# Kernel tuning notes

Hardware: AMD Instinct MI355X
Metric: run time of the kernel (lower is better)

The kernel has to match this reference:

```python
import jax, jax.numpy as jnp
import numpy as np

IN_DIM, HID_DIM, OUT_DIM = 1024, 2048, 1024
DEG1, DEG2 = 8, 8
BATCH = 16384


def cheby_kan_layer(x, coeffs):
    """x: [b, i]; coeffs: [i, o, d+1] -> [b, o].
    Per-feature min-max normalize over batch to [-1,1], Chebyshev recurrence, contract."""
    degree = coeffs.shape[-1] - 1
    mn = jnp.min(x, axis=0, keepdims=True)
    mx = jnp.max(x, axis=0, keepdims=True)
    x = 2.0 * (x - mn) / (mx - mn) - 1.0
    Ts = [jnp.ones_like(x)]
    if degree > 0:
        Ts.append(x)
    for _ in range(2, degree + 1):
        Ts.append(2.0 * x * Ts[-1] - Ts[-2])
    cheby = jnp.stack(Ts, axis=-1)  # [b, i, d+1]
    return jnp.einsum('bid,iod->bo', cheby, coeffs)


def setup_inputs() -> dict:
    key = jax.random.key(0)
    k1, k2, k3 = jax.random.split(key, 3)
    x = jax.random.normal(k1, (BATCH, IN_DIM), dtype=jnp.float32)
    # kaiming-uniform-ish init for coeffs
    b1 = float(np.sqrt(6.0 / IN_DIM))
    b2 = float(np.sqrt(6.0 / HID_DIM))
    coeffs1 = jax.random.uniform(k2, (IN_DIM, HID_DIM, DEG1 + 1), dtype=jnp.float32, minval=-b1, maxval=b1)
    coeffs2 = jax.random.uniform(k3, (HID_DIM, OUT_DIM, DEG2 + 1), dtype=jnp.float32, minval=-b2, maxval=b2)
    return {"x": x, "coeffs1": coeffs1, "coeffs2": coeffs2}


def reference(x, coeffs1, coeffs2):
    h = cheby_kan_layer(x, coeffs1)
    y = cheby_kan_layer(h, coeffs2)
    return y
```

## Files before the change

### kernel.cpp

```cpp
#include <hip/hip_runtime.h>
#include <hip/hip_bf16.h>
#include <stdint.h>


constexpr int BATCH   = 16384;
constexpr int IN_DIM  = 1024;
constexpr int HID_DIM = 2048;
constexpr int OUT_DIM = 1024;
#define DP1 9

using bf16_t = __hip_bfloat16;

typedef __attribute__((ext_vector_type(4))) float f32x4;
typedef __attribute__((ext_vector_type(8))) short s16x8;

static __device__ __forceinline__ unsigned int f2bf_u(float f) {
  union { __hip_bfloat16 h; unsigned short u; } cv;
  cv.h = __float2bfloat16(f);
  return (unsigned int)cv.u;
}

template <typename T>
__global__ void kan_minmax_partial(const T* __restrict__ x, int rows, int cols,
                                   float* __restrict__ mnp, float* __restrict__ mxp) {
  const int c  = blockIdx.x * 64 + (threadIdx.x & 63);
  const int rg = threadIdx.x >> 6;
  const int P  = gridDim.y;
  const int chunk = rows / P;
  const int r0 = blockIdx.y * chunk;
  float mn = 1e30f, mx = -1e30f;
  for (int r = r0 + rg; r < r0 + chunk; r += 4) {
    float v = (float)x[(size_t)r * cols + c];
    mn = fminf(mn, v); mx = fmaxf(mx, v);
  }
  __shared__ float smn[256], smx[256];
  smn[threadIdx.x] = mn; smx[threadIdx.x] = mx;
  __syncthreads();
  if (rg == 0) {
    int t = threadIdx.x;
    mn = fminf(fminf(smn[t], smn[t + 64]), fminf(smn[t + 128], smn[t + 192]));
    mx = fmaxf(fmaxf(smx[t], smx[t + 64]), fmaxf(smx[t + 128], smx[t + 192]));
    mnp[(size_t)blockIdx.y * cols + c] = mn;
    mxp[(size_t)blockIdx.y * cols + c] = mx;
  }
}

__global__ void kan_minmax_finalize(const float* __restrict__ mnp, const float* __restrict__ mxp,
                                    int cols, int P, float* __restrict__ s, float* __restrict__ t) {
  int c = blockIdx.x * blockDim.x + threadIdx.x;
  if (c >= cols) return;
  float mn = 1e30f, mx = -1e30f;
  for (int p = 0; p < P; ++p) {
    mn = fminf(mn, mnp[(size_t)p * cols + c]);
    mx = fmaxf(mx, mxp[(size_t)p * cols + c]);
  }
  float inv = 2.0f / (mx - mn);
  s[c] = inv;
  t[c] = -mn * inv - 1.0f;
}

__global__ void kan_repack(const float* __restrict__ coeffs, int I, int O,
                           bf16_t* __restrict__ Bp) {
  const int NIB = I / 32;
  const int slab = blockIdx.x;
  const int d  = slab % 9;
  const int t2 = slab / 9;
  const int ib = t2 % NIB;
  const int ntile = t2 / NIB;
  for (int c = threadIdx.x; c < 1024; c += 256) {
    const int l16  = c & 15;
    const int quad = (c >> 4) & 3;
    const int ng   = c >> 6;
    const int o = ntile * 256 + ng * 16 + l16;
    const int ibase = ib * 32 + quad * 8;
    unsigned int pk[4];
#pragma unroll
    for (int q = 0; q < 4; ++q) {
      float v0 = coeffs[((size_t)(ibase + 2 * q + 0) * O + o) * DP1 + d];
      float v1 = coeffs[((size_t)(ibase + 2 * q + 1) * O + o) * DP1 + d];
      pk[q] = f2bf_u(v0) | (f2bf_u(v1) << 16);
    }
    *reinterpret_cast<uint4*>(reinterpret_cast<char*>(Bp) +
        ((size_t)slab * 8192 + (size_t)c * 8) * 2) = make_uint4(pk[0], pk[1], pk[2], pk[3]);
  }
}

template <typename AT, typename OT>
__launch_bounds__(256, 2)
__global__ void kan_cheby_gemm(const AT* __restrict__ X, const bf16_t* __restrict__ Bp,
                               const float* __restrict__ sc, const float* __restrict__ tc,
                               OT* __restrict__ out, int I, int N) {
  __shared__ __align__(16) short Als[4096];
  __shared__ __align__(16) short Bls[2][8192];

  const int m0   = blockIdx.x * 128;
  const int n0   = blockIdx.y * 256;
  const int tid  = threadIdx.x;
  const int lane = tid & 63;
  const int wave = tid >> 6;
  const int wr   = wave >> 1;
  const int wc   = wave & 1;
  const int wm4  = wr * 4;
  const int wn16 = wc * 8;
  const int quad = lane >> 4;
  const int l16  = lane & 15;

  const int ma = tid & 127;
  const int hf = tid >> 7;

  const int NIB = I / 32;
  const int nstage = NIB * 9;
  const size_t slab_base = (size_t)blockIdx.y * NIB * 9 * 8192;

  auto dma_b = [&](int ss) {
    const char* g = reinterpret_cast<const char*>(Bp + slab_base + (size_t)ss * 8192) +
                    wave * 4096 + lane * 16;
    char* l = reinterpret_cast<char*>(&Bls[ss & 1][0]) + wave * 4096;
#pragma unroll
    for (int t = 0; t < 4; ++t)
      __builtin_amdgcn_global_load_lds(
          (const __attribute__((address_space(1))) void*)(g + t * 1024),
          (__attribute__((address_space(3))) void*)(l + t * 1024), 16, 0, 0);
  };

  f32x4 acc[4][8] = {};
  float xv[16], Tm1[16], Tm2[16];
#pragma unroll
  for (int j = 0; j < 16; ++j) { xv[j] = 0.f; Tm1[j] = 0.f; Tm2[j] = 0.f; }

  dma_b(0);

  int ib = 0, d = 0;
  for (int s = 0; s < nstage; ++s) {
    __syncthreads();

    if (d == 0) {
      const int fbase = ib * 32 + hf * 16;
      const AT* xp = X + (size_t)(m0 + ma) * I + fbase;
      if constexpr (sizeof(AT) == 4) {
        const float4* p4 = reinterpret_cast<const float4*>(xp);
#pragma unroll
        for (int v = 0; v < 4; ++v) {
          float4 f = p4[v];
          xv[4 * v + 0] = f.x; xv[4 * v + 1] = f.y;
          xv[4 * v + 2] = f.z; xv[4 * v + 3] = f.w;
        }
      } else {
        const uint4* p4 = reinterpret_cast<const uint4*>(xp);
#pragma unroll
        for (int v = 0; v < 2; ++v) {
          uint4 u = p4[v];
          unsigned int wv[4] = {u.x, u.y, u.z, u.w};
#pragma unroll
          for (int q = 0; q < 4; ++q) {
            xv[8 * v + 2 * q + 0] = __uint_as_float(wv[q] << 16);
            xv[8 * v + 2 * q + 1] = __uint_as_float(wv[q] & 0xffff0000u);
          }
        }
      }
      const float4* sp = reinterpret_cast<const float4*>(sc + fbase);
      const float4* tp = reinterpret_cast<const float4*>(tc + fbase);
#pragma unroll
      for (int v = 0; v < 4; ++v) {
        float4 sv = sp[v], tv4 = tp[v];
        xv[4 * v + 0] = fmaf(xv[4 * v + 0], sv.x, tv4.x);
        xv[4 * v + 1] = fmaf(xv[4 * v + 1], sv.y, tv4.y);
        xv[4 * v + 2] = fmaf(xv[4 * v + 2], sv.z, tv4.z);
        xv[4 * v + 3] = fmaf(xv[4 * v + 3], sv.w, tv4.w);
      }
    }

    {
      float tv[16];
      if (d == 0) {
#pragma unroll
        for (int j = 0; j < 16; ++j) tv[j] = 1.0f;
      } else if (d == 1) {
#pragma unroll
        for (int j = 0; j < 16; ++j) tv[j] = xv[j];
      } else {
#pragma unroll
        for (int j = 0; j < 16; ++j) tv[j] = fmaf(2.0f * xv[j], Tm1[j], -Tm2[j]);
      }
#pragma unroll
      for (int j = 0; j < 16; ++j) { Tm2[j] = Tm1[j]; Tm1[j] = tv[j]; }

      unsigned int pk[8];
#pragma unroll
      for (int q = 0; q < 8; ++q)
        pk[q] = f2bf_u(tv[2 * q]) | (f2bf_u(tv[2 * q + 1]) << 16);
      char* b = reinterpret_cast<char*>(Als) +
                (ma >> 4) * 1024 + hf * 512 + (ma & 15) * 16;
      *reinterpret_cast<uint4*>(b)       = make_uint4(pk[0], pk[1], pk[2], pk[3]);
      *reinterpret_cast<uint4*>(b + 256) = make_uint4(pk[4], pk[5], pk[6], pk[7]);
    }

    __syncthreads();

    if (s + 1 < nstage) dma_b(s + 1);

    {
      const char* Ab = reinterpret_cast<const char*>(Als) + lane * 16;
      const char* Bb = reinterpret_cast<const char*>(&Bls[s & 1][0]) + lane * 16;
      s16x8 fa[4], fb[8];
#pragma unroll
      for (int mt = 0; mt < 4; ++mt)
        fa[mt] = *reinterpret_cast<const s16x8*>(Ab + (wm4 + mt) * 1024);
#pragma unroll
      for (int nt = 0; nt < 8; ++nt)
        fb[nt] = *reinterpret_cast<const s16x8*>(Bb + (wn16 + nt) * 1024);
#pragma unroll
      for (int mt = 0; mt < 4; ++mt)
#pragma unroll
        for (int nt = 0; nt < 8; ++nt)
          acc[mt][nt] = __builtin_amdgcn_mfma_f32_16x16x32_bf16(
              fa[mt], fb[nt], acc[mt][nt], 0, 0, 0);
    }

    if (++d == DP1) { d = 0; ++ib; }
  }

#pragma unroll
  for (int mt = 0; mt < 4; ++mt) {
#pragma unroll
    for (int nt = 0; nt < 8; ++nt) {
      const int n = n0 + wc * 128 + nt * 16 + l16;
#pragma unroll
      for (int r = 0; r < 4; ++r) {
        const int m = m0 + wr * 64 + mt * 16 + quad * 4 + r;
        float v = acc[mt][nt][r];
        if constexpr (sizeof(OT) == 4)
          out[(size_t)m * N + n] = v;
        else
          out[(size_t)m * N + n] = __float2bfloat16(v);
      }
    }
  }
}

extern "C" void kernel_launch(void* const* d_in, const int* in_sizes, int n_in,
                              void* d_out, int out_size, void* d_ws, size_t ws_size,
                              hipStream_t stream) {
  const float* x  = (const float*)d_in[0];
  const float* c1 = (const float*)d_in[1];
  const float* c2 = (const float*)d_in[2];
  float* out = (float*)d_out;

  char* ws = (char*)d_ws;
  size_t off = 0;
  auto take = [&](size_t n) -> char* {
    char* p = ws + off;
    off += (n + 255) & ~(size_t)255;
    return p;
  };
  bf16_t* Bp1 = (bf16_t*)take((size_t)HID_DIM * IN_DIM  * DP1 * 2);
  bf16_t* Bp2 = (bf16_t*)take((size_t)OUT_DIM * HID_DIM * DP1 * 2);
  bf16_t* h   = (bf16_t*)take((size_t)BATCH * HID_DIM * 2);
  float* s1  = (float*)take(IN_DIM  * 4);
  float* t1  = (float*)take(IN_DIM  * 4);
  float* s2  = (float*)take(HID_DIM * 4);
  float* t2  = (float*)take(HID_DIM * 4);
  float* mnp = (float*)take((size_t)16 * HID_DIM * 4);
  float* mxp = (float*)take((size_t)16 * HID_DIM * 4);

  kan_minmax_partial<float><<<dim3(IN_DIM / 64, 16), 256, 0, stream>>>(x, BATCH, IN_DIM, mnp, mxp);
  kan_minmax_finalize<<<dim3(IN_DIM / 256), 256, 0, stream>>>(mnp, mxp, IN_DIM, 16, s1, t1);
  kan_repack<<<dim3((HID_DIM / 256) * (IN_DIM / 32) * 9), 256, 0, stream>>>(c1, IN_DIM, HID_DIM, Bp1);
  kan_repack<<<dim3((OUT_DIM / 256) * (HID_DIM / 32) * 9), 256, 0, stream>>>(c2, HID_DIM, OUT_DIM, Bp2);
  kan_cheby_gemm<float, bf16_t><<<dim3(BATCH / 128, HID_DIM / 256), 256, 0, stream>>>(
      x, Bp1, s1, t1, h, IN_DIM, HID_DIM);

  kan_minmax_partial<bf16_t><<<dim3(HID_DIM / 64, 16), 256, 0, stream>>>(h, BATCH, HID_DIM, mnp, mxp);
  kan_minmax_finalize<<<dim3(HID_DIM / 256), 256, 0, stream>>>(mnp, mxp, HID_DIM, 16, s2, t2);
  kan_cheby_gemm<bf16_t, float><<<dim3(BATCH / 128, OUT_DIM / 256), 256, 0, stream>>>(
      h, Bp2, s2, t2, out, HID_DIM, OUT_DIM);
}
```

Measured before the change: 2.216 ms.

## Double-buffer A tile, prefetch X, single barrier per stage, and coalesce repack

The GEMM now double-buffers the Chebyshev A tile in LDS and builds stage s+1's A operand (and issues the B DMA) before running stage s's MFMAs. This cuts two barriers per stage to one and overlaps the basis computation with the matrix work. Raw X loads for the next feature block are prefetched into registers, and the bf16 conversion uses a vector convertvector. The repack kernel reads all 9 degrees per coefficient contiguously, where it previously did 9 strided passes. In exchange it uses more LDS and registers, which may hurt the 2-blocks-per-CU occupancy.

```diff
diff --git a/kernel.cpp b/kernel.cpp
--- a/kernel.cpp
+++ b/kernel.cpp
@@ -13,6 +13,8 @@
 
 typedef __attribute__((ext_vector_type(4))) float f32x4;
 typedef __attribute__((ext_vector_type(8))) short s16x8;
+typedef __attribute__((ext_vector_type(16))) float f32x16;
+typedef __attribute__((ext_vector_type(16))) __bf16 bf16x16;
 
 static __device__ __forceinline__ unsigned int f2bf_u(float f) {
   union { __hip_bfloat16 h; unsigned short u; } cv;
@@ -62,26 +64,32 @@
 __global__ void kan_repack(const float* __restrict__ coeffs, int I, int O,
                            bf16_t* __restrict__ Bp) {
   const int NIB = I / 32;
-  const int slab = blockIdx.x;
-  const int d  = slab % 9;
-  const int t2 = slab / 9;
-  const int ib = t2 % NIB;
-  const int ntile = t2 / NIB;
+  const int ib = blockIdx.x % NIB;
+  const int ntile = blockIdx.x / NIB;
+  const size_t slab0 = (size_t)(ntile * NIB + ib) * 9 * 8192;
   for (int c = threadIdx.x; c < 1024; c += 256) {
     const int l16  = c & 15;
     const int quad = (c >> 4) & 3;
     const int ng   = c >> 6;
     const int o = ntile * 256 + ng * 16 + l16;
     const int ibase = ib * 32 + quad * 8;
-    unsigned int pk[4];
-#pragma unroll
-    for (int q = 0; q < 4; ++q) {
-      float v0 = coeffs[((size_t)(ibase + 2 * q + 0) * O + o) * DP1 + d];
-      float v1 = coeffs[((size_t)(ibase + 2 * q + 1) * O + o) * DP1 + d];
-      pk[q] = f2bf_u(v0) | (f2bf_u(v1) << 16);
-    }
-    *reinterpret_cast<uint4*>(reinterpret_cast<char*>(Bp) +
-        ((size_t)slab * 8192 + (size_t)c * 8) * 2) = make_uint4(pk[0], pk[1], pk[2], pk[3]);
+    float v[8][9];
+#pragma unroll
+    for (int q = 0; q < 8; ++q) {
+      const float* rp = coeffs + ((size_t)(ibase + q) * O + o) * DP1;
+#pragma unroll
+      for (int d = 0; d < 9; ++d) v[q][d] = rp[d];
+    }
+#pragma unroll
+    for (int d = 0; d < 9; ++d) {
+      unsigned int pk[4];
+#pragma unroll
+      for (int q = 0; q < 4; ++q)
+        pk[q] = f2bf_u(v[2 * q][d]) | (f2bf_u(v[2 * q + 1][d]) << 16);
+      *reinterpret_cast<uint4*>(reinterpret_cast<char*>(Bp) +
+          (slab0 + (size_t)d * 8192 + (size_t)c * 8) * 2) =
+          make_uint4(pk[0], pk[1], pk[2], pk[3]);
+    }
   }
 }
 
@@ -90,11 +98,10 @@
 __global__ void kan_cheby_gemm(const AT* __restrict__ X, const bf16_t* __restrict__ Bp,
                                const float* __restrict__ sc, const float* __restrict__ tc,
                                OT* __restrict__ out, int I, int N) {
-  __shared__ __align__(16) short Als[4096];
+  __shared__ __align__(16) short Als[2][4096];
   __shared__ __align__(16) short Bls[2][8192];
 
   const int m0   = blockIdx.x * 128;
-  const int n0   = blockIdx.y * 256;
   const int tid  = threadIdx.x;
   const int lane = tid & 63;
   const int wave = tid >> 6;
@@ -123,84 +130,95 @@
           (__attribute__((address_space(3))) void*)(l + t * 1024), 16, 0, 0);
   };
 
+  uint4 rq[4];
+  auto load_raw = [&](int ibx) {
+    const char* xp = reinterpret_cast<const char*>(
+        X + (size_t)(m0 + ma) * I + ibx * 32 + hf * 16);
+    if constexpr (sizeof(AT) == 4) {
+      rq[0] = *reinterpret_cast<const uint4*>(xp +  0);
+      rq[1] = *reinterpret_cast<const uint4*>(xp + 16);
+      rq[2] = *reinterpret_cast<const uint4*>(xp + 32);
+      rq[3] = *reinterpret_cast<const uint4*>(xp + 48);
+    } else {
+      rq[0] = *reinterpret_cast<const uint4*>(xp +  0);
+      rq[1] = *reinterpret_cast<const uint4*>(xp + 16);
+    }
+  };
+
+  f32x16 xv, Tm1, Tm2;
+#pragma unroll
+  for (int j = 0; j < 16; ++j) { xv[j] = 0.f; Tm1[j] = 0.f; Tm2[j] = 0.f; }
+
+  auto unpack_norm = [&](int ibx) {
+    const int fbase = ibx * 32 + hf * 16;
+    float rv[16];
+    const unsigned int* w = reinterpret_cast<const unsigned int*>(rq);
+    if constexpr (sizeof(AT) == 4) {
+#pragma unroll
+      for (int j = 0; j < 16; ++j) rv[j] = __uint_as_float(w[j]);
+    } else {
+#pragma unroll
+      for (int q = 0; q < 8; ++q) {
+        rv[2 * q + 0] = __uint_as_float(w[q] << 16);
+        rv[2 * q + 1] = __uint_as_float(w[q] & 0xffff0000u);
+      }
+    }
+    const float4* sp = reinterpret_cast<const float4*>(sc + fbase);
+    const float4* tp = reinterpret_cast<const float4*>(tc + fbase);
+#pragma unroll
+    for (int v = 0; v < 4; ++v) {
+      float4 s4 = sp[v], t4 = tp[v];
+      xv[4 * v + 0] = fmaf(rv[4 * v + 0], s4.x, t4.x);
+      xv[4 * v + 1] = fmaf(rv[4 * v + 1], s4.y, t4.y);
+      xv[4 * v + 2] = fmaf(rv[4 * v + 2], s4.z, t4.z);
+      xv[4 * v + 3] = fmaf(rv[4 * v + 3], s4.w, t4.w);
+    }
+  };
+
+  auto write_a = [&](int buf, const f32x16& tv) {
+    union { bf16x16 v; uint4 q[2]; } u;
+    u.v = __builtin_convertvector(tv, bf16x16);
+    char* b = reinterpret_cast<char*>(&Als[buf][0]) +
+              (ma >> 4) * 1024 + hf * 512 + (ma & 15) * 16;
+    *reinterpret_cast<uint4*>(b)       = u.q[0];
+    *reinterpret_cast<uint4*>(b + 256) = u.q[1];
+  };
+
   f32x4 acc[4][8] = {};
-  float xv[16], Tm1[16], Tm2[16];
-#pragma unroll
-  for (int j = 0; j < 16; ++j) { xv[j] = 0.f; Tm1[j] = 0.f; Tm2[j] = 0.f; }
-
+
+  load_raw(0);
   dma_b(0);
-
-  int ib = 0, d = 0;
+  {
+    f32x16 ones;
+#pragma unroll
+    for (int j = 0; j < 16; ++j) ones[j] = 1.0f;
+    write_a(0, ones);
+    Tm1 = ones;
+  }
+  __syncthreads();
+
+  int dn = 1, ibn = 0;
   for (int s = 0; s < nstage; ++s) {
-    __syncthreads();
-
-    if (d == 0) {
-      const int fbase = ib * 32 + hf * 16;
-      const AT* xp = X + (size_t)(m0 + ma) * I + fbase;
-      if constexpr (sizeof(AT) == 4) {
-        const float4* p4 = reinterpret_cast<const float4*>(xp);
-#pragma unroll
-        for (int v = 0; v < 4; ++v) {
-          float4 f = p4[v];
-          xv[4 * v + 0] = f.x; xv[4 * v + 1] = f.y;
-          xv[4 * v + 2] = f.z; xv[4 * v + 3] = f.w;
-        }
+    if (s + 1 < nstage) {
+      dma_b(s + 1);
+      f32x16 tv;
+      if (dn == 0) {
+#pragma unroll
+        for (int j = 0; j < 16; ++j) tv[j] = 1.0f;
+      } else if (dn == 1) {
+        unpack_norm(ibn);
+        if (ibn + 1 < NIB) load_raw(ibn + 1);
+        tv = xv;
       } else {
-        const uint4* p4 = reinterpret_cast<const uint4*>(xp);
-#pragma unroll
-        for (int v = 0; v < 2; ++v) {
-          uint4 u = p4[v];
-          unsigned int wv[4] = {u.x, u.y, u.z, u.w};
-#pragma unroll
-          for (int q = 0; q < 4; ++q) {
-            xv[8 * v + 2 * q + 0] = __uint_as_float(wv[q] << 16);
-            xv[8 * v + 2 * q + 1] = __uint_as_float(wv[q] & 0xffff0000u);
-          }
-        }
+        tv = 2.0f * xv * Tm1 - Tm2;
       }
-      const float4* sp = reinterpret_cast<const float4*>(sc + fbase);
-      const float4* tp = reinterpret_cast<const float4*>(tc + fbase);
-#pragma unroll
-      for (int v = 0; v < 4; ++v) {
-        float4 sv = sp[v], tv4 = tp[v];
-        xv[4 * v + 0] = fmaf(xv[4 * v + 0], sv.x, tv4.x);
-        xv[4 * v + 1] = fmaf(xv[4 * v + 1], sv.y, tv4.y);
-        xv[4 * v + 2] = fmaf(xv[4 * v + 2], sv.z, tv4.z);
-        xv[4 * v + 3] = fmaf(xv[4 * v + 3], sv.w, tv4.w);
-      }
+      Tm2 = Tm1; Tm1 = tv;
+      write_a((s + 1) & 1, tv);
+      if (++dn == DP1) { dn = 0; ++ibn; }
     }
 
     {
-      float tv[16];
-      if (d == 0) {
-#pragma unroll
-        for (int j = 0; j < 16; ++j) tv[j] = 1.0f;
-      } else if (d == 1) {
-#pragma unroll
-        for (int j = 0; j < 16; ++j) tv[j] = xv[j];
-      } else {
-#pragma unroll
-        for (int j = 0; j < 16; ++j) tv[j] = fmaf(2.0f * xv[j], Tm1[j], -Tm2[j]);
-      }
-#pragma unroll
-      for (int j = 0; j < 16; ++j) { Tm2[j] = Tm1[j]; Tm1[j] = tv[j]; }
-
-      unsigned int pk[8];
-#pragma unroll
-      for (int q = 0; q < 8; ++q)
-        pk[q] = f2bf_u(tv[2 * q]) | (f2bf_u(tv[2 * q + 1]) << 16);
-      char* b = reinterpret_cast<char*>(Als) +
-                (ma >> 4) * 1024 + hf * 512 + (ma & 15) * 16;
-      *reinterpret_cast<uint4*>(b)       = make_uint4(pk[0], pk[1], pk[2], pk[3]);
-      *reinterpret_cast<uint4*>(b + 256) = make_uint4(pk[4], pk[5], pk[6], pk[7]);
-    }
-
-    __syncthreads();
-
-    if (s + 1 < nstage) dma_b(s + 1);
-
-    {
-      const char* Ab = reinterpret_cast<const char*>(Als) + lane * 16;
+      const char* Ab = reinterpret_cast<const char*>(&Als[s & 1][0]) + lane * 16;
       const char* Bb = reinterpret_cast<const char*>(&Bls[s & 1][0]) + lane * 16;
       s16x8 fa[4], fb[8];
 #pragma unroll
@@ -217,9 +235,10 @@
               fa[mt], fb[nt], acc[mt][nt], 0, 0, 0);
     }
 
-    if (++d == DP1) { d = 0; ++ib; }
-  }
-
+    __syncthreads();
+  }
+
+  const int n0 = blockIdx.y * 256;
 #pragma unroll
   for (int mt = 0; mt < 4; ++mt) {
 #pragma unroll
@@ -265,8 +284,8 @@
 
   kan_minmax_partial<float><<<dim3(IN_DIM / 64, 16), 256, 0, stream>>>(x, BATCH, IN_DIM, mnp, mxp);
   kan_minmax_finalize<<<dim3(IN_DIM / 256), 256, 0, stream>>>(mnp, mxp, IN_DIM, 16, s1, t1);
-  kan_repack<<<dim3((HID_DIM / 256) * (IN_DIM / 32) * 9), 256, 0, stream>>>(c1, IN_DIM, HID_DIM, Bp1);
-  kan_repack<<<dim3((OUT_DIM / 256) * (HID_DIM / 32) * 9), 256, 0, stream>>>(c2, HID_DIM, OUT_DIM, Bp2);
+  kan_repack<<<dim3((HID_DIM / 256) * (IN_DIM / 32)), 256, 0, stream>>>(c1, IN_DIM, HID_DIM, Bp1);
+  kan_repack<<<dim3((OUT_DIM / 256) * (HID_DIM / 32)), 256, 0, stream>>>(c2, HID_DIM, OUT_DIM, Bp2);
   kan_cheby_gemm<float, bf16_t><<<dim3(BATCH / 128, HID_DIM / 256), 256, 0, stream>>>(
       x, Bp1, s1, t1, h, IN_DIM, HID_DIM);
 
```

Result: faster. 1.868 ms (-15.7%).
